# Kernel tuning notes

Hardware: AMD Instinct MI355X
Metric: run time of the kernel (lower is better)

The kernel has to match this reference:

```python
import jax, jax.numpy as jnp
import numpy as np

THRESHOLD = 0.9
EPS = 1e-12


def setup_inputs() -> dict:
    key = jax.random.key(0)
    ks = jax.random.split(key, 7)
    B, D_in, H1, H2, D_out = 8192, 256, 512, 256, 64
    # torch Linear default init ~ U(-1/sqrt(fan_in), 1/sqrt(fan_in)); randn scaled is fine as a stand-in
    def lin(k, out_f, in_f):
        return jax.random.normal(k, (out_f, in_f), dtype=jnp.float32) / np.sqrt(in_f)
    return {
        "x": jax.random.normal(ks[0], (B, D_in), dtype=jnp.float32),
        "W1": lin(ks[1], H1, D_in),
        "b1": jax.random.normal(ks[2], (H1,), dtype=jnp.float32) * 0.01,
        "W2": lin(ks[3], H2, H1),
        "b2": jax.random.normal(ks[4], (H2,), dtype=jnp.float32) * 0.01,
        "W3": lin(ks[5], D_out, H2),
        "b3": jax.random.normal(ks[6], (D_out,), dtype=jnp.float32) * 0.01,
    }


def reference(x, W1, b1, W2, b2, W3, b3):
    # MLP: Linear -> Tanh -> Linear -> Tanh -> Linear (no tanh on last)
    h1 = jnp.tanh(x @ W1.T + b1)          # [B, 512]
    h2 = jnp.tanh(h1 @ W2.T + b2)         # [B, 256]
    out = h2 @ W3.T + b3                  # [B, 64]

    # Pairwise state fidelity: (normalized dot)^2, thresholded adjacency (diag excluded)
    norms = jnp.linalg.norm(out, axis=-1, keepdims=True)  # [B, 1]
    normed = out / (norms + EPS)
    fid = (normed @ normed.T) ** 2                         # [B, B]
    adj = (fid >= THRESHOLD).astype(out.dtype)
    B = out.shape[0]
    adj = adj * (1.0 - jnp.eye(B, dtype=out.dtype))        # no self-edges (i < j pairs only)

    return adj @ out                                       # [B, 64]
```

## Files before the change

kernel.cpp:

```cpp
#include <hip/hip_runtime.h>
#include <hip/hip_bf16.h>
#include <math.h>

#define B_ROWS 8192
#define D_IN   256
#define H1_DIM 512
#define H2_DIM 256
#define D_OUT  64
#define EPSF   1e-12f
#define THRESH 0.9f
#define BAND_LO 0.89f
#define BAND_HI 0.91f

typedef __attribute__((ext_vector_type(8))) short short8;
typedef __attribute__((ext_vector_type(4))) float f32x4;

__device__ inline float tanh_fast(float xx) {
  const float ax = fabsf(xx);
  const float t = __expf(-2.0f * ax);
  const float r = (1.0f - t) / (1.0f + t);
  return xx < 0.0f ? -r : r;
}

__device__ inline void splitf8(float4 a, float4 b, short8& h, short8& m) {
  float v[8] = {a.x, a.y, a.z, a.w, b.x, b.y, b.z, b.w};
  short h8[8], m8[8];
#pragma unroll
  for (int e = 0; e < 8; ++e) {
    __hip_bfloat16 hb = __float2bfloat16(v[e]);
    float hf = __bfloat162float(hb);
    __hip_bfloat16 mb = __float2bfloat16(v[e] - hf);
    h8[e] = *(short*)&hb;
    m8[e] = *(short*)&mb;
  }
  h = *(short8*)h8;
  m = *(short8*)m8;
}

__device__ inline void rd8_swz(const float* buf, int S, int row, int kl,
                               float4& a, float4& b) {
  const int xr = (row & 7) << 2;
  a = *(const float4*)&buf[(row * S + kl) ^ xr];
  b = *(const float4*)&buf[(row * S + kl + 4) ^ xr];
}

__device__ inline void pack8(const float* __restrict__ src, short* __restrict__ dh,
                             short* __restrict__ dm, int t, int C, int lgq) {
  const int lane = t & 63;
  const int g = t >> 6;
  const int q = g & ((1 << lgq) - 1);
  const int I = g >> lgq;
  const int row = I * 16 + (lane & 15);
  const int k0 = q * 32 + ((lane >> 4) << 3);
  const float* p = src + (size_t)row * C + k0;
  short8 hh, mm;
  splitf8(*(const float4*)p, *(const float4*)(p + 4), hh, mm);
  *(short8*)(dh + (size_t)t * 8) = hh;
  *(short8*)(dm + (size_t)t * 8) = mm;
}

__global__ __launch_bounds__(256)
void wpack(const float* __restrict__ W1, const float* __restrict__ W2,
           const float* __restrict__ W3,
           short* w1h, short* w1m, short* w2h, short* w2m,
           short* w3h, short* w3m) {
  const int b = blockIdx.x, tid = threadIdx.x;
  if (b < 64)        pack8(W1, w1h, w1m, b * 256 + tid, 256, 3);
  else if (b < 128)  pack8(W2, w2h, w2m, (b - 64) * 256 + tid, 512, 4);
  else               pack8(W3, w3h, w3m, (b - 128) * 256 + tid, 256, 3);
}

__global__ __launch_bounds__(512, 4)
void fused_mlp16(const float* __restrict__ x,
                 const short* __restrict__ w1h, const short* __restrict__ w1m,
                 const float* __restrict__ b1,
                 const short* __restrict__ w2h, const short* __restrict__ w2m,
                 const float* __restrict__ b2,
                 const short* __restrict__ w3h, const short* __restrict__ w3m,
                 const float* __restrict__ b3,
                 float* __restrict__ out, short* __restrict__ vph,
                 short* __restrict__ vpm, float* __restrict__ res) {
  __shared__ __align__(16) char smem[49152];
  short* xph   = (short*)smem;
  short* xpm   = (short*)(smem + 8192);
  float* wbuf1 = (float*)smem;
  float* wbuf3 = (float*)smem;
  short* h1h   = (short*)(smem + 16384);
  short* h1m   = (short*)(smem + 32768);
  float* wbuf2 = (float*)(smem + 16384);
  short* h2ph  = (short*)(smem + 32768);
  short* h2pm  = (short*)(smem + 40960);
  __shared__ float nsum[16];
  __shared__ float invn[16];

  const int tid = threadIdx.x;
  const int wave = tid >> 6, lane = tid & 63;
  const int r0 = blockIdx.x * 16;
  const int col16 = lane & 15;
  const int rbase = (lane >> 4) << 2;

  if (tid < 256) {
    float4* rz = (float4*)(res + (size_t)r0 * D_OUT);
    rz[tid] = make_float4(0.f, 0.f, 0.f, 0.f);
  }

  {
    const int lu = tid & 63, q = tid >> 6;
    const float* p = x + (size_t)(r0 + (lu & 15)) * D_IN + q * 32 + ((lu >> 4) << 3);
    short8 hh, mm;
    splitf8(*(const float4*)p, *(const float4*)(p + 4), hh, mm);
    const int off = (q * 64 + lu) * 8;
    *(short8*)(xph + off) = hh;
    *(short8*)(xpm + off) = mm;
  }
  __syncthreads();

  f32x4 acc1[4];
#pragma unroll
  for (int jj = 0; jj < 4; ++jj) acc1[jj] = (f32x4){0.f, 0.f, 0.f, 0.f};
#pragma unroll 4
  for (int q = 0; q < 8; ++q) {
    const int aoff = (q * 64 + lane) * 8;
    const short8 Ah = *(const short8*)(xph + aoff);
    const short8 Am = *(const short8*)(xpm + aoff);
#pragma unroll
    for (int jj = 0; jj < 4; ++jj) {
      const int boff = (((wave * 4 + jj) * 8 + q) * 64 + lane) * 8;
      const short8 Bh = *(const short8*)(w1h + boff);
      const short8 Bm = *(const short8*)(w1m + boff);
      acc1[jj] = __builtin_amdgcn_mfma_f32_16x16x32_bf16(Ah, Bh, acc1[jj], 0, 0, 0);
      acc1[jj] = __builtin_amdgcn_mfma_f32_16x16x32_bf16(Ah, Bm, acc1[jj], 0, 0, 0);
      acc1[jj] = __builtin_amdgcn_mfma_f32_16x16x32_bf16(Am, Bh, acc1[jj], 0, 0, 0);
    }
  }
  __syncthreads();

  float bv1[4];
#pragma unroll
  for (int jj = 0; jj < 4; ++jj) bv1[jj] = b1[(wave * 4 + jj) * 16 + col16];
#pragma unroll
  for (int h = 0; h < 2; ++h) {
    if ((wave >> 2) == h) {
#pragma unroll
      for (int jj = 0; jj < 4; ++jj)
#pragma unroll
        for (int r = 0; r < 4; ++r) {
          const int row = rbase + r;
          const int col = ((wave & 3) * 4 + jj) * 16 + col16;
          wbuf1[(row * 256 + col) ^ ((row & 7) << 2)] = tanh_fast(acc1[jj][r] + bv1[jj]);
        }
    }
    __syncthreads();
    {
      const int lu = tid & 63, ql = tid >> 6;
      const int row = lu & 15, kl = ql * 32 + ((lu >> 4) << 3);
      float4 a, b;
      rd8_swz(wbuf1, 256, row, kl, a, b);
      short8 hh, mm;
      splitf8(a, b, hh, mm);
      const int off = ((h * 8 + ql) * 64 + lu) * 8;
      *(short8*)(h1h + off) = hh;
      *(short8*)(h1m + off) = mm;
    }
    __syncthreads();
  }

  f32x4 acc2[2];
#pragma unroll
  for (int jj = 0; jj < 2; ++jj) acc2[jj] = (f32x4){0.f, 0.f, 0.f, 0.f};
#pragma unroll 4
  for (int q = 0; q < 16; ++q) {
    const int aoff = (q * 64 + lane) * 8;
    const short8 Ah = *(const short8*)(h1h + aoff);
    const short8 Am = *(const short8*)(h1m + aoff);
#pragma unroll
    for (int jj = 0; jj < 2; ++jj) {
      const int boff = (((wave * 2 + jj) * 16 + q) * 64 + lane) * 8;
      const short8 Bh = *(const short8*)(w2h + boff);
      const short8 Bm = *(const short8*)(w2m + boff);
      acc2[jj] = __builtin_amdgcn_mfma_f32_16x16x32_bf16(Ah, Bh, acc2[jj], 0, 0, 0);
      acc2[jj] = __builtin_amdgcn_mfma_f32_16x16x32_bf16(Ah, Bm, acc2[jj], 0, 0, 0);
      acc2[jj] = __builtin_amdgcn_mfma_f32_16x16x32_bf16(Am, Bh, acc2[jj], 0, 0, 0);
    }
  }
  __syncthreads();

  {
    float bv2[2];
#pragma unroll
    for (int jj = 0; jj < 2; ++jj) bv2[jj] = b2[(wave * 2 + jj) * 16 + col16];
#pragma unroll
    for (int jj = 0; jj < 2; ++jj)
#pragma unroll
      for (int r = 0; r < 4; ++r) {
        const int row = rbase + r;
        const int col = (wave * 2 + jj) * 16 + col16;
        wbuf2[(row * 256 + col) ^ ((row & 7) << 2)] = tanh_fast(acc2[jj][r] + bv2[jj]);
      }
  }
  __syncthreads();
  {
    const int lu = tid & 63, ql = tid >> 6;
    const int row = lu & 15, kl = ql * 32 + ((lu >> 4) << 3);
    float4 a, b;
    rd8_swz(wbuf2, 256, row, kl, a, b);
    short8 hh, mm;
    splitf8(a, b, hh, mm);
    const int off = (ql * 64 + lu) * 8;
    *(short8*)(h2ph + off) = hh;
    *(short8*)(h2pm + off) = mm;
  }
  __syncthreads();

  if (wave < 4) {
    f32x4 acc3 = (f32x4){0.f, 0.f, 0.f, 0.f};
#pragma unroll 4
    for (int q = 0; q < 8; ++q) {
      const int aoff = (q * 64 + lane) * 8;
      const short8 Ah = *(const short8*)(h2ph + aoff);
      const short8 Am = *(const short8*)(h2pm + aoff);
      const int boff = ((wave * 8 + q) * 64 + lane) * 8;
      const short8 Bh = *(const short8*)(w3h + boff);
      const short8 Bm = *(const short8*)(w3m + boff);
      acc3 = __builtin_amdgcn_mfma_f32_16x16x32_bf16(Ah, Bh, acc3, 0, 0, 0);
      acc3 = __builtin_amdgcn_mfma_f32_16x16x32_bf16(Ah, Bm, acc3, 0, 0, 0);
      acc3 = __builtin_amdgcn_mfma_f32_16x16x32_bf16(Am, Bh, acc3, 0, 0, 0);
    }
    const float bv3 = b3[wave * 16 + col16];
#pragma unroll
    for (int r = 0; r < 4; ++r) {
      const int row = rbase + r;
      const int col = wave * 16 + col16;
      wbuf3[(row * 64 + col) ^ ((row & 7) << 2)] = acc3[r] + bv3;
    }
  }
  __syncthreads();

  if (tid < 256) {
    const int row = tid >> 4, c4 = (tid & 15) * 4;
    const float4 a = *(const float4*)&wbuf3[(row * 64 + c4) ^ ((row & 7) << 2)];
    float s = a.x * a.x + a.y * a.y + a.z * a.z + a.w * a.w;
    s += __shfl_xor(s, 1, 64);
    s += __shfl_xor(s, 2, 64);
    s += __shfl_xor(s, 4, 64);
    s += __shfl_xor(s, 8, 64);
    if ((tid & 15) == 0) nsum[row] = s;
  }
  __syncthreads();
  if (tid < 16) invn[tid] = 1.0f / (sqrtf(nsum[tid]) + EPSF);
  __syncthreads();

  if (tid < 256) {
    const int row = tid >> 4, c4 = (tid & 15) * 4;
    *(float4*)(out + (size_t)(r0 + row) * D_OUT + c4) =
        *(const float4*)&wbuf3[(row * 64 + c4) ^ ((row & 7) << 2)];
  }
  if (tid < 128) {
    const int lu = tid & 63, ql = tid >> 6;
    const int row = lu & 15, kl = ql * 32 + ((lu >> 4) << 3);
    const float sc = invn[row];
    float4 a, b;
    rd8_swz(wbuf3, 64, row, kl, a, b);
    a.x *= sc; a.y *= sc; a.z *= sc; a.w *= sc;
    b.x *= sc; b.y *= sc; b.z *= sc; b.w *= sc;
    short8 hh, mm;
    splitf8(a, b, hh, mm);
    const size_t off = (((size_t)blockIdx.x * 2 + ql) * 64 + lu) * 8;
    *(short8*)(vph + off) = hh;
    *(short8*)(vpm + off) = mm;
  }
}

__global__ __launch_bounds__(256, 2)
void gram_accum(const short* __restrict__ vph, const short* __restrict__ vpm,
                const float* __restrict__ out, float* __restrict__ res) {
  __shared__ __align__(16) short lAh[8 * 1024];
  const int tid = threadIdx.x;
  const int wave = tid >> 6, lane = tid & 63;

  const int t = blockIdx.x;
  int I = (int)((129.0f - sqrtf(16641.0f - 8.0f * (float)t)) * 0.5f);
  if (I < 0) I = 0;
  while (64 * (I + 1) - ((I + 1) * I) / 2 <= t) ++I;
  while (64 * I - (I * (I - 1)) / 2 > t) --I;
  const int Jc = I + (t - (64 * I - (I * (I - 1)) / 2));
  const int i0 = I * 128;
  const int j0c = Jc * 128;

  {
    const size_t base = (size_t)I * 8192;
#pragma unroll
    for (int u = 0; u < 4; ++u) {
      const int item = wave * 4 + u;
      __builtin_amdgcn_global_load_lds(
          (const __attribute__((address_space(1))) void*)(vph + base + item * 512 + lane * 8),
          (__attribute__((address_space(3))) void*)(lAh + item * 512), 16, 0, 0);
    }
  }
  __syncthreads();

  short8 Ah[8][2];
#pragma unroll
  for (int it = 0; it < 8; ++it)
#pragma unroll
    for (int q = 0; q < 2; ++q)
      Ah[it][q] = *(const short8*)(lAh + it * 1024 + q * 512 + lane * 8);

#pragma unroll
  for (int tt = 0; tt < 2; ++tt) {
    const int jt = wave * 2 + tt;
    const int j0 = j0c + jt * 16;
    const short* jb_h = vph + (size_t)(j0 >> 4) * 1024;
    short8 Bh0 = *(const short8*)(jb_h + lane * 8);
    short8 Bh1 = *(const short8*)(jb_h + 512 + lane * 8);

    f32x4 g[8];
#pragma unroll
    for (int it = 0; it < 8; ++it) g[it] = (f32x4){0.f, 0.f, 0.f, 0.f};
#pragma unroll
    for (int it = 0; it < 8; ++it) g[it] = __builtin_amdgcn_mfma_f32_16x16x32_bf16(Ah[it][0], Bh0, g[it], 0, 0, 0);
#pragma unroll
    for (int it = 0; it < 8; ++it) g[it] = __builtin_amdgcn_mfma_f32_16x16x32_bf16(Ah[it][1], Bh1, g[it], 0, 0, 0);

    bool band = false;
#pragma unroll
    for (int it = 0; it < 8; ++it)
#pragma unroll
      for (int r = 0; r < 4; ++r) {
        const float f = g[it][r] * g[it][r];
        band = band || (f > BAND_LO && f < BAND_HI);
      }
    if (__any(band)) {
      const short* jb_m = vpm + (size_t)(j0 >> 4) * 1024;
      short8 Bm0 = *(const short8*)(jb_m + lane * 8);
      short8 Bm1 = *(const short8*)(jb_m + 512 + lane * 8);
#pragma unroll
      for (int it = 0; it < 8; ++it) g[it] = __builtin_amdgcn_mfma_f32_16x16x32_bf16(Ah[it][0], Bm0, g[it], 0, 0, 0);
#pragma unroll
      for (int it = 0; it < 8; ++it) g[it] = __builtin_amdgcn_mfma_f32_16x16x32_bf16(Ah[it][1], Bm1, g[it], 0, 0, 0);
#pragma unroll
      for (int it = 0; it < 8; ++it) {
        const size_t abase = (size_t)((i0 >> 4) + it) * 1024;
        short8 Am0 = *(const short8*)(vpm + abase + lane * 8);
        short8 Am1 = *(const short8*)(vpm + abase + 512 + lane * 8);
        g[it] = __builtin_amdgcn_mfma_f32_16x16x32_bf16(Am0, Bh0, g[it], 0, 0, 0);
        g[it] = __builtin_amdgcn_mfma_f32_16x16x32_bf16(Am1, Bh1, g[it], 0, 0, 0);
      }
    }

    const int jl = j0 + (lane & 15);
#pragma unroll
    for (int it = 0; it < 8; ++it)
#pragma unroll
      for (int r = 0; r < 4; ++r) {
        const int il = i0 + it * 16 + (lane >> 4) * 4 + r;
        unsigned long long m =
            __ballot((g[it][r] * g[it][r] >= THRESH) && (il < jl));
        while (m) {
          const int s = __builtin_ctzll(m);
          m &= m - 1;
          const int js = j0 + (s & 15);
          const int is = i0 + it * 16 + ((s >> 4) << 2) + r;
          atomicAdd(res + (size_t)is * D_OUT + lane, out[(size_t)js * D_OUT + lane]);
          atomicAdd(res + (size_t)js * D_OUT + lane, out[(size_t)is * D_OUT + lane]);
        }
      }
  }
}

#define MB (1024 * 1024)
#define KB 1024

extern "C" void kernel_launch(void* const* d_in, const int* in_sizes, int n_in,
                              void* d_out, int out_size, void* d_ws, size_t ws_size,
                              hipStream_t stream) {
  const float* x  = (const float*)d_in[0];
  const float* W1 = (const float*)d_in[1];
  const float* b1 = (const float*)d_in[2];
  const float* W2 = (const float*)d_in[3];
  const float* b2 = (const float*)d_in[4];
  const float* W3 = (const float*)d_in[5];
  const float* b3 = (const float*)d_in[6];
  float* res = (float*)d_out;

  char* ws = (char*)d_ws;
  float* out = (float*)(ws);
  short* vph = (short*)(ws + 2 * MB);
  short* vpm = (short*)(ws + 3 * MB);
  short* w1h = (short*)(ws + 4 * MB);
  short* w1m = (short*)(ws + 4 * MB + 256 * KB);
  short* w2h = (short*)(ws + 4 * MB + 512 * KB);
  short* w2m = (short*)(ws + 4 * MB + 768 * KB);
  short* w3h = (short*)(ws + 5 * MB);
  short* w3m = (short*)(ws + 5 * MB + 32 * KB);

  wpack<<<136, 256, 0, stream>>>(W1, W2, W3, w1h, w1m, w2h, w2m, w3h, w3m);
  fused_mlp16<<<512, 512, 0, stream>>>(x, w1h, w1m, b1, w2h, w2m, b2,
                                       w3h, w3m, b3, out, vph, vpm, res);
  gram_accum<<<dim3(2080), 256, 0, stream>>>(vph, vpm, out, res);
}
```

Baseline: 117.9 us.

## Stage A hi/lo in LDS and always apply split-bf16 correction in gram

The gram kernel now loads both the high and low bf16 parts of the A tile into LDS and reads A operands from LDS on demand instead of holding them in registers. It drops the near-threshold band check and always runs the full three-term split-bf16 product. The intent is to cut register pressure and remove the divergent global loads of the correction operand. The cost is extra MFMA work on every tile, where the old version only did it for tiles near the threshold. The ballot now fires for all off-diagonal hits, and the i<j filter moves inside the loop, which adds scalar iterations that do no work.

```diff
diff --git a/kernel.cpp b/kernel.cpp
--- a/kernel.cpp
+++ b/kernel.cpp
@@ -9,8 +9,6 @@
 #define D_OUT  64
 #define EPSF   1e-12f
 #define THRESH 0.9f
-#define BAND_LO 0.89f
-#define BAND_HI 0.91f
 
 typedef __attribute__((ext_vector_type(8))) short short8;
 typedef __attribute__((ext_vector_type(4))) float f32x4;
@@ -275,6 +273,7 @@
 void gram_accum(const short* __restrict__ vph, const short* __restrict__ vpm,
                 const float* __restrict__ out, float* __restrict__ res) {
   __shared__ __align__(16) short lAh[8 * 1024];
+  __shared__ __align__(16) short lAm[8 * 1024];
   const int tid = threadIdx.x;
   const int wave = tid >> 6, lane = tid & 63;
 
@@ -290,62 +289,62 @@
   {
     const size_t base = (size_t)I * 8192;
 #pragma unroll
-    for (int u = 0; u < 4; ++u) {
-      const int item = wave * 4 + u;
+    for (int u = 0; u < 8; ++u) {
+      const int item = wave * 8 + u;
+      const short* src;
+      short* dst;
+      if (item < 16) { src = vph + base + item * 512; dst = lAh + item * 512; }
+      else           { src = vpm + base + (item - 16) * 512; dst = lAm + (item - 16) * 512; }
       __builtin_amdgcn_global_load_lds(
-          (const __attribute__((address_space(1))) void*)(vph + base + item * 512 + lane * 8),
-          (__attribute__((address_space(3))) void*)(lAh + item * 512), 16, 0, 0);
-    }
-  }
-  __syncthreads();
-
-  short8 Ah[8][2];
-#pragma unroll
-  for (int it = 0; it < 8; ++it)
-#pragma unroll
-    for (int q = 0; q < 2; ++q)
-      Ah[it][q] = *(const short8*)(lAh + it * 1024 + q * 512 + lane * 8);
+          (const __attribute__((address_space(1))) void*)(src + lane * 8),
+          (__attribute__((address_space(3))) void*)dst, 16, 0, 0);
+    }
+  }
+  __syncthreads();
 
 #pragma unroll
   for (int tt = 0; tt < 2; ++tt) {
     const int jt = wave * 2 + tt;
     const int j0 = j0c + jt * 16;
     const short* jb_h = vph + (size_t)(j0 >> 4) * 1024;
+    const short* jb_m = vpm + (size_t)(j0 >> 4) * 1024;
     short8 Bh0 = *(const short8*)(jb_h + lane * 8);
     short8 Bh1 = *(const short8*)(jb_h + 512 + lane * 8);
+    short8 Bm0 = *(const short8*)(jb_m + lane * 8);
+    short8 Bm1 = *(const short8*)(jb_m + 512 + lane * 8);
 
     f32x4 g[8];
 #pragma unroll
     for (int it = 0; it < 8; ++it) g[it] = (f32x4){0.f, 0.f, 0.f, 0.f};
 #pragma unroll
-    for (int it = 0; it < 8; ++it) g[it] = __builtin_amdgcn_mfma_f32_16x16x32_bf16(Ah[it][0], Bh0, g[it], 0, 0, 0);
-#pragma unroll
-    for (int it = 0; it < 8; ++it) g[it] = __builtin_amdgcn_mfma_f32_16x16x32_bf16(Ah[it][1], Bh1, g[it], 0, 0, 0);
-
-    bool band = false;
-#pragma unroll
-    for (int it = 0; it < 8; ++it)
-#pragma unroll
-      for (int r = 0; r < 4; ++r) {
-        const float f = g[it][r] * g[it][r];
-        band = band || (f > BAND_LO && f < BAND_HI);
-      }
-    if (__any(band)) {
-      const short* jb_m = vpm + (size_t)(j0 >> 4) * 1024;
-      short8 Bm0 = *(const short8*)(jb_m + lane * 8);
-      short8 Bm1 = *(const short8*)(jb_m + 512 + lane * 8);
-#pragma unroll
-      for (int it = 0; it < 8; ++it) g[it] = __builtin_amdgcn_mfma_f32_16x16x32_bf16(Ah[it][0], Bm0, g[it], 0, 0, 0);
-#pragma unroll
-      for (int it = 0; it < 8; ++it) g[it] = __builtin_amdgcn_mfma_f32_16x16x32_bf16(Ah[it][1], Bm1, g[it], 0, 0, 0);
-#pragma unroll
-      for (int it = 0; it < 8; ++it) {
-        const size_t abase = (size_t)((i0 >> 4) + it) * 1024;
-        short8 Am0 = *(const short8*)(vpm + abase + lane * 8);
-        short8 Am1 = *(const short8*)(vpm + abase + 512 + lane * 8);
-        g[it] = __builtin_amdgcn_mfma_f32_16x16x32_bf16(Am0, Bh0, g[it], 0, 0, 0);
-        g[it] = __builtin_amdgcn_mfma_f32_16x16x32_bf16(Am1, Bh1, g[it], 0, 0, 0);
-      }
+    for (int it = 0; it < 8; ++it) {
+      const short8 A0 = *(const short8*)(lAh + it * 1024 + lane * 8);
+      g[it] = __builtin_amdgcn_mfma_f32_16x16x32_bf16(A0, Bh0, g[it], 0, 0, 0);
+    }
+#pragma unroll
+    for (int it = 0; it < 8; ++it) {
+      const short8 A1 = *(const short8*)(lAh + it * 1024 + 512 + lane * 8);
+      g[it] = __builtin_amdgcn_mfma_f32_16x16x32_bf16(A1, Bh1, g[it], 0, 0, 0);
+    }
+#pragma unroll
+    for (int it = 0; it < 8; ++it) {
+      const short8 A0 = *(const short8*)(lAh + it * 1024 + lane * 8);
+      g[it] = __builtin_amdgcn_mfma_f32_16x16x32_bf16(A0, Bm0, g[it], 0, 0, 0);
+    }
+#pragma unroll
+    for (int it = 0; it < 8; ++it) {
+      const short8 A1 = *(const short8*)(lAh + it * 1024 + 512 + lane * 8);
+      g[it] = __builtin_amdgcn_mfma_f32_16x16x32_bf16(A1, Bm1, g[it], 0, 0, 0);
+    }
+#pragma unroll
+    for (int it = 0; it < 8; ++it) {
+      const short8 M0 = *(const short8*)(lAm + it * 1024 + lane * 8);
+      g[it] = __builtin_amdgcn_mfma_f32_16x16x32_bf16(M0, Bh0, g[it], 0, 0, 0);
+    }
+#pragma unroll
+    for (int it = 0; it < 8; ++it) {
+      const short8 M1 = *(const short8*)(lAm + it * 1024 + 512 + lane * 8);
+      g[it] = __builtin_amdgcn_mfma_f32_16x16x32_bf16(M1, Bh1, g[it], 0, 0, 0);
     }
 
     const int jl = j0 + (lane & 15);
@@ -355,14 +354,16 @@
       for (int r = 0; r < 4; ++r) {
         const int il = i0 + it * 16 + (lane >> 4) * 4 + r;
         unsigned long long m =
-            __ballot((g[it][r] * g[it][r] >= THRESH) && (il < jl));
+            __ballot((g[it][r] * g[it][r] >= THRESH) && (il != jl));
         while (m) {
           const int s = __builtin_ctzll(m);
           m &= m - 1;
           const int js = j0 + (s & 15);
           const int is = i0 + it * 16 + ((s >> 4) << 2) + r;
-          atomicAdd(res + (size_t)is * D_OUT + lane, out[(size_t)js * D_OUT + lane]);
-          atomicAdd(res + (size_t)js * D_OUT + lane, out[(size_t)is * D_OUT + lane]);
+          if (is < js) {
+            atomicAdd(res + (size_t)is * D_OUT + lane, out[(size_t)js * D_OUT + lane]);
+            atomicAdd(res + (size_t)js * D_OUT + lane, out[(size_t)is * D_OUT + lane]);
+          }
         }
       }
   }
```

After: 114.9 us (median of 3 runs). 1.03x faster.
